# Kernel tuning notes

Measured on AMD Instinct MI355X. Metric: run time of the kernel, lower is better.

## Reference

```python
import jax, jax.numpy as jnp
import numpy as np

B, C, N, V, H = 8, 256, 1024, 12, 4
D = C // H  # 64
BN_EPS = 1e-5
NEG = 1e10


def _vconv(x, W, b, g, bt, m4):
    """VointConv block: 1x1 conv + BN(batch stats) + relu, with reset_voint_mask
    applied after every sublayer (as in the torch loop).
    x: [B, Cin, N, V], W: [Cout, Cin], m4: [B, 1, N, V] float mask."""
    y = (jnp.einsum('oc,bcnv->bonv', W, x) + b[None, :, None, None]) * m4
    mu = jnp.mean(y, axis=(0, 2, 3), keepdims=True)
    var = jnp.var(y, axis=(0, 2, 3), keepdims=True)
    y = ((y - mu) * jax.lax.rsqrt(var + BN_EPS) * g[None, :, None, None]
         + bt[None, :, None, None]) * m4
    return jax.nn.relu(y) * m4


def setup_inputs() -> dict:
    key = jax.random.key(0)
    ks = jax.random.split(key, 20)
    inp = {}
    inp['voints_feats'] = jax.random.normal(ks[0], (B, C, N, V), jnp.float32)
    inp['voints_mask'] = (jax.random.uniform(ks[1], (B, N, V)) > 0.3).astype(jnp.float32)
    w = lambda k, shp: (jax.random.normal(k, shp, jnp.float32) * 0.05)
    # embed_layers[0]: VointConv([C, C/heads])
    inp['We'] = w(ks[2], (D, C)); inp['be'] = w(ks[3], (D,))
    inp['ge'] = 1.0 + 0.1 * jax.random.normal(ks[4], (D,), jnp.float32)
    inp['bne'] = 0.1 * jax.random.normal(ks[5], (D,), jnp.float32)
    # embed_atten_layers[0]: VointConv([C/heads, 3*C])
    inp['Wa'] = w(ks[6], (3 * C, D)); inp['ba'] = w(ks[7], (3 * C,))
    inp['ga'] = 1.0 + 0.1 * jax.random.normal(ks[8], (3 * C,), jnp.float32)
    inp['bna'] = 0.1 * jax.random.normal(ks[9], (3 * C,), jnp.float32)
    # to_out[0]: VointConv([C, C])
    inp['Wo'] = w(ks[10], (C, C)); inp['bo'] = w(ks[11], (C,))
    inp['go'] = 1.0 + 0.1 * jax.random.normal(ks[12], (C,), jnp.float32)
    inp['bno'] = 0.1 * jax.random.normal(ks[13], (C,), jnp.float32)
    # feedforward[0]: VointConv([C, C])
    inp['Wf'] = w(ks[14], (C, C)); inp['bf'] = w(ks[15], (C,))
    inp['gf'] = 1.0 + 0.1 * jax.random.normal(ks[16], (C,), jnp.float32)
    inp['bnf'] = 0.1 * jax.random.normal(ks[17], (C,), jnp.float32)
    return inp


def reference(voints_feats, voints_mask, We, be, ge, bne, Wa, ba, ga, bna,
              Wo, bo, go, bno, Wf, bf, gf, bnf):
    mask = voints_mask                      # [B, N, V] float
    m4 = mask[:, None, :, :]                # [B, 1, N, V]
    # embedding to per-head dim, then joint QKV projection
    emb = _vconv(voints_feats, We, be, ge, bne, m4)      # [B, D, N, V]
    qkv = _vconv(emb, Wa, ba, ga, bna, m4)               # [B, 3C, N, V]
    k, q, v = jnp.split(qkv, 3, axis=1)                  # torch.chunk order: k, q, v
    resh = lambda t: t.reshape(B, H, D, N, V)            # 'b (h d) n v -> b h d n v'
    q, k, v = resh(q), resh(k), resh(v)
    scale = float(C) ** (-0.5)
    dots = jnp.einsum('bhdnv,bhdnj->bhnvj', q, k) * scale  # [B,H,N,V,V]
    empty = jnp.sum(mask, axis=-1) == 0                  # [B, N]
    dots = jnp.where(empty[:, None, :, None, None], 0.0, dots)
    # vointsoftmax: bias broadcasts over query dim v (mask[...,None] -> [B,1,N,V,1])
    qbias = jnp.where(mask[:, None, :, :, None] > 0, 0.0, -NEG)
    attn = jax.nn.softmax(dots + qbias, axis=-1) * mask[:, None, :, :, None]
    # faithful to source: 'b h n v j, b h d n v -> b h n v d' (j summed over attn only)
    out = jnp.einsum('bhnvj,bhdnv->bhnvd', attn, v)      # [B,H,N,V,D]
    out = out.transpose(0, 1, 4, 2, 3).reshape(B, C, N, V)  # 'b h n v d -> b (h d) n v'
    out = jnp.where(empty[:, None, :, None], 0.0, out)
    out = _vconv(out, Wo, bo, go, bno, m4)
    x = voints_feats + out
    x = x + _vconv(x, Wf, bf, gf, bnf, m4)
    return x
```

## Files before the change

### kernel.cpp

```cpp
#include <hip/hip_runtime.h>
#include <hip/hip_bf16.h>

typedef __attribute__((ext_vector_type(8))) __bf16 bf16x8;
typedef __attribute__((ext_vector_type(4))) float floatx4;
typedef __attribute__((ext_vector_type(8))) unsigned short ushort8;

namespace {
constexpr int kC  = 256;
constexpr int kNV = 1024 * 12;
constexpr int kP  = 8 * kNV;
constexpr float kEps = 1e-5f;

constexpr size_t OFF_PARAMS = 0;
constexpr size_t OFF_PART   = 2048;
constexpr size_t OFF_WB     = 2048 + 16384;
constexpr size_t OFF_XT     = OFF_WB + 81920;
constexpr size_t OFF_Y1     = OFF_XT + (size_t)kP * 256 / 2;
constexpr size_t OFF_Y2     = OFF_Y1 + (size_t)kP * 64 / 2;
constexpr size_t OFF_Y3     = OFF_Y2 + (size_t)kP * 256 / 2;
}

__device__ __forceinline__ unsigned short f2bf(float f) {
    unsigned int u = __builtin_bit_cast(unsigned int, f);
    u += 0x7FFFu + ((u >> 16) & 1u);
    return (unsigned short)(u >> 16);
}
__device__ __forceinline__ float bf2f(unsigned short h) {
    unsigned int u = ((unsigned int)h) << 16;
    return __builtin_bit_cast(float, u);
}

__global__ void convw_kernel(const float* __restrict__ We, const float* __restrict__ Wa,
                             const float* __restrict__ Wo, const float* __restrict__ Wf,
                             unsigned short* __restrict__ dst)
{
    const int f = (blockIdx.x * 256 + threadIdx.x) * 4;
    const float* src; int off, M, K, base;
    if (f < 16384)      { src = We;            off = f;         M = 64;  K = 256; base = 0; }
    else if (f < 32768) { src = Wa + 512 * 64; off = f - 16384; M = 256; K = 64;  base = 16384; }
    else if (f < 98304) { src = Wo;            off = f - 32768; M = 256; K = 256; base = 32768; }
    else                { src = Wf;            off = f - 98304; M = 256; K = 256; base = 98304; }
    const int m = off / K, k = off - m * K;
    const float4 v = *(const float4*)&src[off];
    ushort4 o; o.x = f2bf(v.x); o.y = f2bf(v.y); o.z = f2bf(v.z); o.w = f2bf(v.w);
    *(ushort4*)&dst[base + (k >> 5) * (M * 32) + m * 32 + (k & 31)] = o;
}

__global__ __launch_bounds__(256) void transpose_kernel(
    const float* __restrict__ x, unsigned short* __restrict__ xT)
{
    __shared__ float T[64][65];
    const int p0 = blockIdx.x * 64;
    const int c0 = blockIdx.y * 64;
    const int b  = p0 / kNV;
    const int q0 = p0 - b * kNV;
    const int t  = threadIdx.x;

    const int cl = t >> 2;
    const int pq = (t & 3) * 16;
    const float* src = &x[(size_t)(b * kC + c0 + cl) * kNV + q0 + pq];
    #pragma unroll
    for (int i = 0; i < 4; ++i) {
        const float4 v = *(const float4*)&src[i * 4];
        T[cl][pq + i * 4 + 0] = v.x;
        T[cl][pq + i * 4 + 1] = v.y;
        T[cl][pq + i * 4 + 2] = v.z;
        T[cl][pq + i * 4 + 3] = v.w;
    }
    __syncthreads();
    const int pr = t >> 2;
    const int cb = (t & 3) * 16;
    #pragma unroll
    for (int i = 0; i < 2; ++i) {
        ushort8 o;
        #pragma unroll
        for (int j = 0; j < 8; ++j) o[j] = f2bf(T[cb + i * 8 + j][pr]);
        *(ushort8*)&xT[(size_t)(p0 + pr) * 256 + c0 + cb + i * 8] = o;
    }
}

template<int MODE>
__device__ __forceinline__ ushort8 xform(ushort8 y8, ushort8 x8, float mp,
                                         const float* __restrict__ actA,
                                         const float* __restrict__ actB, int kk)
{
    if constexpr (MODE == 0) {
        return y8;
    } else {
        const float4 a0 = *(const float4*)&actA[kk];
        const float4 a1 = *(const float4*)&actA[kk + 4];
        const float4 b0 = *(const float4*)&actB[kk];
        const float4 b1 = *(const float4*)&actB[kk + 4];
        const float aa[8] = {a0.x, a0.y, a0.z, a0.w, a1.x, a1.y, a1.z, a1.w};
        const float bb[8] = {b0.x, b0.y, b0.z, b0.w, b1.x, b1.y, b1.z, b1.w};
        ushort8 o;
        #pragma unroll
        for (int j = 0; j < 8; ++j) {
            float v = bf2f(y8[j]);
            v = mp * fmaxf(fmaf(aa[j], v, bb[j]), 0.f);
            if constexpr (MODE == 2) v += bf2f(x8[j]);
            o[j] = f2bf(v);
        }
        return o;
    }
}

template<int BM, int K, int MODE>
__global__ __launch_bounds__(256, 2) void gemm_kernel(
    const unsigned short* __restrict__ Apk, const float* __restrict__ bias,
    const unsigned short* __restrict__ Yprev, unsigned short* __restrict__ XT,
    const float* __restrict__ mask,
    const float* __restrict__ actA, const float* __restrict__ actB,
    unsigned short* __restrict__ Yout, float* __restrict__ partial, int slabsPerBlock)
{
    constexpr int LD = 264;
    constexpr int NT = K / 32;
    constexpr int FM = BM / 64;
    constexpr int FP = 2;
    constexpr int CH = K / 64;
    __shared__ unsigned short Bs[2][32 * LD];
    __shared__ float Sst[2][256];

    const int tid  = threadIdx.x;
    const int w    = tid >> 6, lane = tid & 63, quad = lane >> 4, lt = lane & 15;
    const int mBase = w * 16 * FM;

    Sst[0][tid] = 0.f; Sst[1][tid] = 0.f;

    ushort8 Areg[NT][FM];
    #pragma unroll
    for (int t = 0; t < NT; ++t)
        #pragma unroll
        for (int fm = 0; fm < FM; ++fm)
            Areg[t][fm] = *(const ushort8*)&Apk[(size_t)(t * BM + mBase + fm * 16 + lt) * 32 + quad * 8];

    const int spb   = slabsPerBlock;
    const int slab0 = blockIdx.x * spb;

    {
        const int pBase = slab0 * 32;
        #pragma unroll
        for (int i = 0; i < CH; ++i) {
            const int c = tid + i * 256;
            const int p = c / (K / 8);
            const int kq = (c % (K / 8)) * 8;
            const ushort8 y8 = *(const ushort8*)&Yprev[(size_t)(pBase + p) * K + kq];
            ushort8 o;
            if constexpr (MODE == 0) o = y8;
            else {
                ushort8 x8{};
                if constexpr (MODE == 2) x8 = *(const ushort8*)&XT[(size_t)(pBase + p) * K + kq];
                o = xform<MODE>(y8, x8, mask[pBase + p], actA, actB, kq);
                if constexpr (MODE == 2) *(ushort8*)&XT[(size_t)(pBase + p) * K + kq] = o;
            }
            *(ushort8*)&Bs[0][p * LD + kq] = o;
        }
    }
    __syncthreads();

    for (int s = 0; s < spb; ++s) {
        const int pBase = (slab0 + s) * 32;
        const bool hasNext = (s + 1 < spb);

        ushort8 py[CH];
        ushort8 px[(MODE == 2) ? CH : 1];
        if (hasNext) {
            const int pN = (slab0 + s + 1) * 32;
            #pragma unroll
            for (int i = 0; i < CH; ++i) {
                const int c = tid + i * 256;
                const int p = c / (K / 8);
                const int kq = (c % (K / 8)) * 8;
                py[i] = *(const ushort8*)&Yprev[(size_t)(pN + p) * K + kq];
                if constexpr (MODE == 2)
                    px[i] = *(const ushort8*)&XT[(size_t)(pN + p) * K + kq];
            }
        }

        floatx4 acc[FM][FP];
        #pragma unroll
        for (int fm = 0; fm < FM; ++fm)
            #pragma unroll
            for (int fp = 0; fp < FP; ++fp) acc[fm][fp] = (floatx4)0.f;

        const unsigned short* bs = &Bs[s & 1][0];
        #pragma unroll
        for (int t = 0; t < NT; ++t) {
            bf16x8 bF[FP];
            #pragma unroll
            for (int fp = 0; fp < FP; ++fp)
                bF[fp] = *(const bf16x8*)&bs[(fp * 16 + lt) * LD + t * 32 + quad * 8];
            #pragma unroll
            for (int fm = 0; fm < FM; ++fm) {
                const bf16x8 aF = __builtin_bit_cast(bf16x8, Areg[t][fm]);
                #pragma unroll
                for (int fp = 0; fp < FP; ++fp)
                    acc[fm][fp] = __builtin_amdgcn_mfma_f32_16x16x32_bf16(aF, bF[fp], acc[fm][fp], 0, 0, 0);
            }
        }

        float mpv[FP];
        #pragma unroll
        for (int fp = 0; fp < FP; ++fp) mpv[fp] = mask[pBase + fp * 16 + lt];

        float sS[FM][4], sQ[FM][4];
        #pragma unroll
        for (int fm = 0; fm < FM; ++fm)
            #pragma unroll
            for (int i = 0; i < 4; ++i) { sS[fm][i] = 0.f; sQ[fm][i] = 0.f; }

        #pragma unroll
        for (int fm = 0; fm < FM; ++fm) {
            const float4 bia = *(const float4*)&bias[mBase + fm * 16 + quad * 4];
            const float bi[4] = {bia.x, bia.y, bia.z, bia.w};
            #pragma unroll
            for (int fp = 0; fp < FP; ++fp) {
                const int pG = pBase + fp * 16 + lt;
                float vv[4];
                #pragma unroll
                for (int i = 0; i < 4; ++i) {
                    const float v = (acc[fm][fp][i] + bi[i]) * mpv[fp];
                    vv[i] = v; sS[fm][i] += v; sQ[fm][i] += v * v;
                }
                ushort4 o; o.x = f2bf(vv[0]); o.y = f2bf(vv[1]); o.z = f2bf(vv[2]); o.w = f2bf(vv[3]);
                *(ushort4*)&Yout[(size_t)pG * BM + mBase + fm * 16 + quad * 4] = o;
            }
        }
        #pragma unroll
        for (int fm = 0; fm < FM; ++fm)
            #pragma unroll
            for (int i = 0; i < 4; ++i) {
                #pragma unroll
                for (int off = 1; off < 16; off <<= 1) {
                    sS[fm][i] += __shfl_xor(sS[fm][i], off);
                    sQ[fm][i] += __shfl_xor(sQ[fm][i], off);
                }
            }
        if (lt == 0) {
            #pragma unroll
            for (int fm = 0; fm < FM; ++fm)
                #pragma unroll
                for (int i = 0; i < 4; ++i) {
                    const int ch = mBase + fm * 16 + quad * 4 + i;
                    Sst[0][ch] += sS[fm][i];
                    Sst[1][ch] += sQ[fm][i];
                }
        }

        if (hasNext) {
            const int pN = (slab0 + s + 1) * 32;
            unsigned short* bn = &Bs[(s + 1) & 1][0];
            #pragma unroll
            for (int i = 0; i < CH; ++i) {
                const int c = tid + i * 256;
                const int p = c / (K / 8);
                const int kq = (c % (K / 8)) * 8;
                ushort8 o;
                if constexpr (MODE == 0) o = py[i];
                else {
                    ushort8 x8{};
                    if constexpr (MODE == 2) x8 = px[i];
                    o = xform<MODE>(py[i], x8, mask[pN + p], actA, actB, kq);
                    if constexpr (MODE == 2) *(ushort8*)&XT[(size_t)(pN + p) * K + kq] = o;
                }
                *(ushort8*)&bn[p * LD + kq] = o;
            }
        }
        __syncthreads();
    }

    if (tid < BM) {
        float* pb = partial + (size_t)(blockIdx.x & 7) * 512;
        atomicAdd(&pb[tid], Sst[0][tid]);
        atomicAdd(&pb[256 + tid], Sst[1][tid]);
    }
}

__global__ void finalize_kernel(const float* __restrict__ part,
                                const float* __restrict__ g, const float* __restrict__ bt,
                                float* __restrict__ ab, int M)
{
    const int m = blockIdx.x * 64 + threadIdx.x;
    if (m >= M) return;
    float s = 0.f, s2 = 0.f;
    #pragma unroll
    for (int k = 0; k < 8; ++k) { s += part[k * 512 + m]; s2 += part[k * 512 + 256 + m]; }
    const float mu  = s * (1.f / kP);
    const float var = s2 * (1.f / kP) - mu * mu;
    const float A = rsqrtf(var + kEps) * g[m];
    ab[m] = A;
    ab[256 + m] = fmaf(-mu, A, bt[m]);
}

__global__ __launch_bounds__(256) void final_kernel(
    const unsigned short* __restrict__ x1, const unsigned short* __restrict__ y4,
    const float* __restrict__ p4, const float* __restrict__ mask, float* __restrict__ out)
{
    constexpr int TL = 264;
    __shared__ unsigned short TX[32 * TL];
    __shared__ unsigned short T4[32 * TL];
    const int p0 = blockIdx.x * 32;
    const int b  = p0 / kNV;
    const int q0 = p0 - b * kNV;

    #pragma unroll
    for (int i = 0; i < 4; ++i) {
        const int idx = threadIdx.x + i * 256;
        const int p = idx >> 5, c0 = (idx & 31) * 8;
        *(ushort8*)&TX[p * TL + c0] = *(const ushort8*)&x1[(size_t)(p0 + p) * 256 + c0];
        *(ushort8*)&T4[p * TL + c0] = *(const ushort8*)&y4[(size_t)(p0 + p) * 256 + c0];
    }
    __syncthreads();

    const int qv = (threadIdx.x & 15) * 2;
    const int cb = threadIdx.x >> 4;
    const float m0v = mask[p0 + qv], m1v = mask[p0 + qv + 1];
    #pragma unroll
    for (int j = 0; j < 16; ++j) {
        const int c = cb + j * 16;
        const float a4 = p4[c], b4 = p4[256 + c];
        const size_t ro = (size_t)(b * kC + c) * kNV + q0 + qv;
        float2 o;
        o.x = bf2f(TX[qv * TL + c])       + m0v * fmaxf(fmaf(a4, bf2f(T4[qv * TL + c]), b4), 0.f);
        o.y = bf2f(TX[(qv + 1) * TL + c]) + m1v * fmaxf(fmaf(a4, bf2f(T4[(qv + 1) * TL + c]), b4), 0.f);
        *(float2*)&out[ro] = o;
    }
}

extern "C" void kernel_launch(void* const* d_in, const int* in_sizes, int n_in,
                              void* d_out, int out_size, void* d_ws, size_t ws_size,
                              hipStream_t stream)
{
    const float* x    = (const float*)d_in[0];
    const float* mask = (const float*)d_in[1];
    const float* We   = (const float*)d_in[2];
    const float* be   = (const float*)d_in[3];
    const float* ge   = (const float*)d_in[4];
    const float* bne  = (const float*)d_in[5];
    const float* Wa   = (const float*)d_in[6];
    const float* ba   = (const float*)d_in[7];
    const float* ga   = (const float*)d_in[8];
    const float* bna  = (const float*)d_in[9];
    const float* Wo   = (const float*)d_in[10];
    const float* bo   = (const float*)d_in[11];
    const float* go   = (const float*)d_in[12];
    const float* bno  = (const float*)d_in[13];
    const float* Wf   = (const float*)d_in[14];
    const float* bf   = (const float*)d_in[15];
    const float* gf   = (const float*)d_in[16];
    const float* bnf  = (const float*)d_in[17];
    float* out = (float*)d_out;
    float* ws  = (float*)d_ws;

    float* params = ws + OFF_PARAMS;
    float* part   = ws + OFF_PART;
    unsigned short* Wb = (unsigned short*)(ws + OFF_WB);
    unsigned short* xT = (unsigned short*)(ws + OFF_XT);
    unsigned short* y1 = (unsigned short*)(ws + OFF_Y1);
    unsigned short* y2 = (unsigned short*)(ws + OFF_Y2);
    unsigned short* y3 = (unsigned short*)(ws + OFF_Y3);

    hipMemsetAsync(part, 0, 16384 * sizeof(float), stream);
    convw_kernel<<<160, 256, 0, stream>>>(We, Wa, Wo, Wf, Wb);
    transpose_kernel<<<dim3(kP / 64, 4), 256, 0, stream>>>(x, xT);

    const dim3 blk(256);
    const dim3 grid(512);
    const int SPB = kP / 32 / 512;

    gemm_kernel<64, 256, 0><<<grid, blk, 0, stream>>>(
        Wb, be, xT, nullptr, mask, nullptr, nullptr, y1, part, SPB);
    finalize_kernel<<<1, 64, 0, stream>>>(part, ge, bne, params, 64);

    gemm_kernel<256, 64, 1><<<grid, blk, 0, stream>>>(
        Wb + 16384, ba + 512, y1, nullptr, mask, params, params + 256, y2, part + 4096, SPB);
    finalize_kernel<<<4, 64, 0, stream>>>(part + 4096, ga + 512, bna + 512, params + 512, 256);

    gemm_kernel<256, 256, 1><<<grid, blk, 0, stream>>>(
        Wb + 32768, bo, y2, nullptr, mask, params + 512, params + 768, y3, part + 8192, SPB);
    finalize_kernel<<<4, 64, 0, stream>>>(part + 8192, go, bno, params + 1024, 256);

    gemm_kernel<256, 256, 2><<<grid, blk, 0, stream>>>(
        Wb + 98304, bf, y3, xT, mask, params + 1024, params + 1280, y2, part + 12288, SPB);
    finalize_kernel<<<4, 64, 0, stream>>>(part + 12288, gf, bnf, params + 1536, 256);

    final_kernel<<<kP / 32, blk, 0, stream>>>(
        xT, y2, params + 1536, mask, out);
}
```

Before: 404.0 us.

## Fold BN finalize into consumer kernels, stream A fragments, raise occupancy

Removes the four separate finalize kernels: each consumer GEMM (and the final kernel) now reduces the partial BN sums itself and puts the scale/shift in shared memory. For the large K=256/BM=256 GEMMs the A-weight fragments are no longer all held in registers but loaded per k-step with one-step prefetch. This cuts VGPR pressure and allows higher launch_bounds occupancy with larger grids (1024 and 768 blocks). The costs are redundant per-block statistic reduction and extra global/L2 reads of weights inside the inner loop.

```diff
diff --git a/kernel.cpp b/kernel.cpp
--- a/kernel.cpp
+++ b/kernel.cpp
@@ -105,12 +105,13 @@
     }
 }
 
-template<int BM, int K, int MODE>
-__global__ __launch_bounds__(256, 2) void gemm_kernel(
+template<int BM, int K, int MODE, int MINW>
+__global__ __launch_bounds__(256, MINW) void gemm_kernel(
     const unsigned short* __restrict__ Apk, const float* __restrict__ bias,
     const unsigned short* __restrict__ Yprev, unsigned short* __restrict__ XT,
     const float* __restrict__ mask,
-    const float* __restrict__ actA, const float* __restrict__ actB,
+    const float* __restrict__ pPrev, const float* __restrict__ gPrev,
+    const float* __restrict__ btPrev,
     unsigned short* __restrict__ Yout, float* __restrict__ partial, int slabsPerBlock)
 {
     constexpr int LD = 264;
@@ -118,8 +119,11 @@
     constexpr int FM = BM / 64;
     constexpr int FP = 2;
     constexpr int CH = K / 64;
+    constexpr bool AREG = (NT * FM <= 8);
     __shared__ unsigned short Bs[2][32 * LD];
     __shared__ float Sst[2][256];
+    __shared__ float ActA[256];
+    __shared__ float ActB[256];
 
     const int tid  = threadIdx.x;
     const int w    = tid >> 6, lane = tid & 63, quad = lane >> 4, lt = lane & 15;
@@ -127,12 +131,33 @@
 
     Sst[0][tid] = 0.f; Sst[1][tid] = 0.f;
 
-    ushort8 Areg[NT][FM];
-    #pragma unroll
-    for (int t = 0; t < NT; ++t)
-        #pragma unroll
-        for (int fm = 0; fm < FM; ++fm)
-            Areg[t][fm] = *(const ushort8*)&Apk[(size_t)(t * BM + mBase + fm * 16 + lt) * 32 + quad * 8];
+    if constexpr (MODE != 0) {
+        if (tid < K) {
+            float s = 0.f, s2 = 0.f;
+            #pragma unroll
+            for (int k = 0; k < 8; ++k) {
+                s  += pPrev[k * 512 + tid];
+                s2 += pPrev[k * 512 + 256 + tid];
+            }
+            const float mu  = s * (1.f / kP);
+            const float var = s2 * (1.f / kP) - mu * mu;
+            const float A   = rsqrtf(var + kEps) * gPrev[tid];
+            ActA[tid] = A;
+            ActB[tid] = fmaf(-mu, A, btPrev[tid]);
+        }
+        __syncthreads();
+    }
+
+    const unsigned short* aBase = &Apk[(size_t)(mBase + lt) * 32 + quad * 8];
+
+    ushort8 Areg[AREG ? NT : 1][FM];
+    if constexpr (AREG) {
+        #pragma unroll
+        for (int t = 0; t < NT; ++t)
+            #pragma unroll
+            for (int fm = 0; fm < FM; ++fm)
+                Areg[t][fm] = *(const ushort8*)&aBase[(size_t)(t * BM + fm * 16) * 32];
+    }
 
     const int spb   = slabsPerBlock;
     const int slab0 = blockIdx.x * spb;
@@ -150,7 +175,7 @@
             else {
                 ushort8 x8{};
                 if constexpr (MODE == 2) x8 = *(const ushort8*)&XT[(size_t)(pBase + p) * K + kq];
-                o = xform<MODE>(y8, x8, mask[pBase + p], actA, actB, kq);
+                o = xform<MODE>(y8, x8, mask[pBase + p], ActA, ActB, kq);
                 if constexpr (MODE == 2) *(ushort8*)&XT[(size_t)(pBase + p) * K + kq] = o;
             }
             *(ushort8*)&Bs[0][p * LD + kq] = o;
@@ -184,18 +209,41 @@
             for (int fp = 0; fp < FP; ++fp) acc[fm][fp] = (floatx4)0.f;
 
         const unsigned short* bs = &Bs[s & 1][0];
+
+        ushort8 aCur[FM];
+        if constexpr (!AREG) {
+            #pragma unroll
+            for (int fm = 0; fm < FM; ++fm)
+                aCur[fm] = *(const ushort8*)&aBase[(size_t)(fm * 16) * 32];
+        }
+
         #pragma unroll
         for (int t = 0; t < NT; ++t) {
             bf16x8 bF[FP];
             #pragma unroll
             for (int fp = 0; fp < FP; ++fp)
                 bF[fp] = *(const bf16x8*)&bs[(fp * 16 + lt) * LD + t * 32 + quad * 8];
+            ushort8 aNxt[FM];
+            if constexpr (!AREG) {
+                if (t + 1 < NT) {
+                    #pragma unroll
+                    for (int fm = 0; fm < FM; ++fm)
+                        aNxt[fm] = *(const ushort8*)&aBase[(size_t)((t + 1) * BM + fm * 16) * 32];
+                }
+            }
             #pragma unroll
             for (int fm = 0; fm < FM; ++fm) {
-                const bf16x8 aF = __builtin_bit_cast(bf16x8, Areg[t][fm]);
+                const bf16x8 aF = AREG ? __builtin_bit_cast(bf16x8, Areg[AREG ? t : 0][fm])
+                                       : __builtin_bit_cast(bf16x8, aCur[fm]);
                 #pragma unroll
                 for (int fp = 0; fp < FP; ++fp)
                     acc[fm][fp] = __builtin_amdgcn_mfma_f32_16x16x32_bf16(aF, bF[fp], acc[fm][fp], 0, 0, 0);
+            }
+            if constexpr (!AREG) {
+                if (t + 1 < NT) {
+                    #pragma unroll
+                    for (int fm = 0; fm < FM; ++fm) aCur[fm] = aNxt[fm];
+                }
             }
         }
 
@@ -260,7 +308,7 @@
                 else {
                     ushort8 x8{};
                     if constexpr (MODE == 2) x8 = px[i];
-                    o = xform<MODE>(py[i], x8, mask[pN + p], actA, actB, kq);
+                    o = xform<MODE>(py[i], x8, mask[pN + p], ActA, ActB, kq);
                     if constexpr (MODE == 2) *(ushort8*)&XT[(size_t)(pN + p) * K + kq] = o;
                 }
                 *(ushort8*)&bn[p * LD + kq] = o;
@@ -276,32 +324,32 @@
     }
 }
 
-__global__ void finalize_kernel(const float* __restrict__ part,
-                                const float* __restrict__ g, const float* __restrict__ bt,
-                                float* __restrict__ ab, int M)
-{
-    const int m = blockIdx.x * 64 + threadIdx.x;
-    if (m >= M) return;
-    float s = 0.f, s2 = 0.f;
-    #pragma unroll
-    for (int k = 0; k < 8; ++k) { s += part[k * 512 + m]; s2 += part[k * 512 + 256 + m]; }
-    const float mu  = s * (1.f / kP);
-    const float var = s2 * (1.f / kP) - mu * mu;
-    const float A = rsqrtf(var + kEps) * g[m];
-    ab[m] = A;
-    ab[256 + m] = fmaf(-mu, A, bt[m]);
-}
-
 __global__ __launch_bounds__(256) void final_kernel(
     const unsigned short* __restrict__ x1, const unsigned short* __restrict__ y4,
-    const float* __restrict__ p4, const float* __restrict__ mask, float* __restrict__ out)
+    const float* __restrict__ part4, const float* __restrict__ g4,
+    const float* __restrict__ bt4,
+    const float* __restrict__ mask, float* __restrict__ out)
 {
     constexpr int TL = 264;
     __shared__ unsigned short TX[32 * TL];
     __shared__ unsigned short T4[32 * TL];
+    __shared__ float PA[256];
+    __shared__ float PB[256];
     const int p0 = blockIdx.x * 32;
     const int b  = p0 / kNV;
     const int q0 = p0 - b * kNV;
+
+    {
+        const int m = threadIdx.x;
+        float s = 0.f, s2 = 0.f;
+        #pragma unroll
+        for (int k = 0; k < 8; ++k) { s += part4[k * 512 + m]; s2 += part4[k * 512 + 256 + m]; }
+        const float mu  = s * (1.f / kP);
+        const float var = s2 * (1.f / kP) - mu * mu;
+        const float A   = rsqrtf(var + kEps) * g4[m];
+        PA[m] = A;
+        PB[m] = fmaf(-mu, A, bt4[m]);
+    }
 
     #pragma unroll
     for (int i = 0; i < 4; ++i) {
@@ -318,7 +366,7 @@
     #pragma unroll
     for (int j = 0; j < 16; ++j) {
         const int c = cb + j * 16;
-        const float a4 = p4[c], b4 = p4[256 + c];
+        const float a4 = PA[c], b4 = PB[c];
         const size_t ro = (size_t)(b * kC + c) * kNV + q0 + qv;
         float2 o;
         o.x = bf2f(TX[qv * TL + c])       + m0v * fmaxf(fmaf(a4, bf2f(T4[qv * TL + c]), b4), 0.f);
@@ -352,8 +400,7 @@
     float* out = (float*)d_out;
     float* ws  = (float*)d_ws;
 
-    float* params = ws + OFF_PARAMS;
-    float* part   = ws + OFF_PART;
+    float* part = ws + OFF_PART;
     unsigned short* Wb = (unsigned short*)(ws + OFF_WB);
     unsigned short* xT = (unsigned short*)(ws + OFF_XT);
     unsigned short* y1 = (unsigned short*)(ws + OFF_Y1);
@@ -365,25 +412,21 @@
     transpose_kernel<<<dim3(kP / 64, 4), 256, 0, stream>>>(x, xT);
 
     const dim3 blk(256);
-    const dim3 grid(512);
-    const int SPB = kP / 32 / 512;
-
-    gemm_kernel<64, 256, 0><<<grid, blk, 0, stream>>>(
-        Wb, be, xT, nullptr, mask, nullptr, nullptr, y1, part, SPB);
-    finalize_kernel<<<1, 64, 0, stream>>>(part, ge, bne, params, 64);
-
-    gemm_kernel<256, 64, 1><<<grid, blk, 0, stream>>>(
-        Wb + 16384, ba + 512, y1, nullptr, mask, params, params + 256, y2, part + 4096, SPB);
-    finalize_kernel<<<4, 64, 0, stream>>>(part + 4096, ga + 512, bna + 512, params + 512, 256);
-
-    gemm_kernel<256, 256, 1><<<grid, blk, 0, stream>>>(
-        Wb + 32768, bo, y2, nullptr, mask, params + 512, params + 768, y3, part + 8192, SPB);
-    finalize_kernel<<<4, 64, 0, stream>>>(part + 8192, go, bno, params + 1024, 256);
-
-    gemm_kernel<256, 256, 2><<<grid, blk, 0, stream>>>(
-        Wb + 98304, bf, y3, xT, mask, params + 1024, params + 1280, y2, part + 12288, SPB);
-    finalize_kernel<<<4, 64, 0, stream>>>(part + 12288, gf, bnf, params + 1536, 256);
+    const int SPB12 = kP / 32 / 1024;
+    const int SPB34 = kP / 32 / 768;
+
+    gemm_kernel<64, 256, 0, 4><<<1024, blk, 0, stream>>>(
+        Wb, be, xT, nullptr, mask, nullptr, nullptr, nullptr, y1, part, SPB12);
+
+    gemm_kernel<256, 64, 1, 4><<<1024, blk, 0, stream>>>(
+        Wb + 16384, ba + 512, y1, nullptr, mask, part, ge, bne, y2, part + 4096, SPB12);
+
+    gemm_kernel<256, 256, 1, 3><<<768, blk, 0, stream>>>(
+        Wb + 32768, bo, y2, nullptr, mask, part + 4096, ga + 512, bna + 512, y3, part + 8192, SPB34);
+
+    gemm_kernel<256, 256, 2, 3><<<768, blk, 0, stream>>>(
+        Wb + 98304, bf, y3, xT, mask, part + 8192, go, bno, y2, part + 12288, SPB34);
 
     final_kernel<<<kP / 32, blk, 0, stream>>>(
-        xT, y2, params + 1536, mask, out);
-}
+        xT, y2, part + 12288, gf, bnf, mask, out);
+}
```

Result: slower. 508.0 us (+25.7%).
